# Optimization experiments

Hardware: AMD Instinct MI355X
Metric: run time of the kernel (lower is better)

Reference implementation:

```python
import jax, jax.numpy as jnp
import numpy as np

N, D, E, OUT = 50000, 256, 320000, 1

def setup_inputs() -> dict:
    key = jax.random.key(0)
    k1, k2, k3, k4, k5, k6 = jax.random.split(key, 6)
    z = jax.random.normal(k1, (N, D), dtype=jnp.float32)
    edge_index = jax.random.randint(k2, (2, E), 0, N, dtype=jnp.int64)
    # xavier_normal for fc1: std = sqrt(2/(fan_in+fan_out)) = sqrt(2/(2D+D))
    w1 = jax.random.normal(k3, (D, 2 * D), dtype=jnp.float32) * np.sqrt(2.0 / (3 * D))
    b1 = jnp.zeros((D,), dtype=jnp.float32)
    w2 = jax.random.normal(k4, (OUT, D), dtype=jnp.float32) * np.sqrt(2.0 / (D + OUT))
    b2 = jnp.zeros((OUT,), dtype=jnp.float32)
    return {"z": z, "edge_index": edge_index, "w1": w1, "b1": b1, "w2": w2, "b2": b2}

def reference(z, edge_index, w1, b1, w2, b2):
    x1 = z[edge_index[0]]                     # [E, D]
    x2 = z[edge_index[1]]                     # [E, D]
    x = jnp.concatenate([x1, x2], axis=1)     # [E, 2D]
    h = jax.nn.relu(x @ w1.T + b1)            # [E, D]
    return h @ w2.T + b2                      # [E, OUT]
```

## Files before the change

### kernel.cpp

```cpp
#include <hip/hip_runtime.h>
#include <hip/hip_bf16.h>

#define D 256
#define TWOD 512
#define BM 128
#define BK 32

typedef __attribute__((ext_vector_type(8))) __bf16 bf16x8;
typedef __attribute__((ext_vector_type(4))) float f32x4;
typedef __attribute__((ext_vector_type(8))) unsigned short ushort8;

using as1_u32 = __attribute__((address_space(1))) const unsigned int;
using as3_u32 = __attribute__((address_space(3))) unsigned int;

__device__ __forceinline__ void gload_lds16(const void* g, void* l) {
    __builtin_amdgcn_global_load_lds((as1_u32*)g, (as3_u32*)l, 16, 0, 0);
}

__device__ __forceinline__ float bf2f(unsigned short u) {
    unsigned int x = ((unsigned int)u) << 16;
    return __uint_as_float(x);
}
__device__ __forceinline__ unsigned short f2bf_bits(float f) {
    unsigned int x = __float_as_uint(f);
    unsigned int r = (x + 0x7fffu + ((x >> 16) & 1u)) >> 16;
    return (unsigned short)r;
}

__global__ __launch_bounds__(256) void wt_conv_kernel(
    const float* __restrict__ w1, unsigned short* __restrict__ Wt)
{
    const int s = blockIdx.x * 256 + threadIdx.x;
    const int j = s >> 9;
    const int kk = s & 511;
    const float v = w1[s];
    const int dst = (kk < D) ? (j * D + kk) : ((D + j) * D + (kk - D));
    Wt[dst] = f2bf_bits(v);
}

__global__ __launch_bounds__(256, 2) void node_proj_mfma(
    const float* __restrict__ z, const unsigned short* __restrict__ Wt,
    unsigned short* __restrict__ C, int M, int Mblocks)
{
    __shared__ __align__(16) float          Abuf[3][BM * BK];
    __shared__ __align__(16) unsigned short Bbuf[3][BM * BK];

    const int bid    = blockIdx.x;
    const int rowblk = (bid >> 5) * 8 + (bid & 7);
    if (rowblk >= Mblocks) return;
    const int m0 = rowblk * BM;
    const int cb = ((bid >> 3) & 3) * BM;

    const int t    = threadIdx.x;
    const int lane = t & 63;
    const int w    = t >> 6;

    const int r16 = lane & 15;
    const int g   = lane >> 4;

    const int wm = (w >> 1) * 64;
    const int wn = (w & 1) * 64;

    f32x4 acc[4][4];
    #pragma unroll
    for (int mt = 0; mt < 4; ++mt)
        #pragma unroll
        for (int nt = 0; nt < 4; ++nt)
            acc[mt][nt] = (f32x4){0.f, 0.f, 0.f, 0.f};

    auto stage = [&](int buf, int k0) {
        #pragma unroll
        for (int i = 0; i < 4; ++i) {
            const int c = i * 256 + t;
            const int r = c >> 3;
            const int q = c & 7;
            const int col = ((q ^ (r & 7)) << 2);
            const int row = min(m0 + r, M - 1);
            const float* gsrc = z + (size_t)row * D + k0 + col;
            float* ldst = &Abuf[buf][(size_t)(i * 256 + w * 64) * 4];
            gload_lds16(gsrc, ldst);
        }
        #pragma unroll
        for (int i = 0; i < 2; ++i) {
            const int c = i * 256 + t;
            const int r = c >> 2;
            const int q = c & 3;
            const int sb = (r ^ (r >> 2)) & 3;
            const int col = ((q ^ sb) << 3);
            const unsigned short* gsrc = Wt + (size_t)(cb + r) * D + k0 + col;
            unsigned short* ldst = &Bbuf[buf][(size_t)(i * 256 + w * 64) * 8];
            gload_lds16(gsrc, ldst);
        }
    };

    auto compute = [&](int buf) {
        bf16x8 b[4];
        #pragma unroll
        for (int nt = 0; nt < 4; ++nt) {
            const int rl = wn + nt * 16 + r16;
            const int sb = (rl ^ (rl >> 2)) & 3;
            const ushort8 bu = *(const ushort8*)&Bbuf[buf][rl * 32 + ((g ^ sb) << 3)];
            b[nt] = __builtin_bit_cast(bf16x8, bu);
        }
        bf16x8 a[4];
        #pragma unroll
        for (int mt = 0; mt < 4; ++mt) {
            const int rl = wm + mt * 16 + r16;
            const int s = rl & 7;
            const f32x4 f0 = *(const f32x4*)&Abuf[buf][rl * 32 + (((2 * g) ^ s) << 2)];
            const f32x4 f1 = *(const f32x4*)&Abuf[buf][rl * 32 + (((2 * g + 1) ^ s) << 2)];
            bf16x8 tt;
            tt[0] = (__bf16)f0[0]; tt[1] = (__bf16)f0[1];
            tt[2] = (__bf16)f0[2]; tt[3] = (__bf16)f0[3];
            tt[4] = (__bf16)f1[0]; tt[5] = (__bf16)f1[1];
            tt[6] = (__bf16)f1[2]; tt[7] = (__bf16)f1[3];
            a[mt] = tt;
        }

        __builtin_amdgcn_s_setprio(1);
        #pragma unroll
        for (int nt = 0; nt < 4; ++nt)
            #pragma unroll
            for (int mt = 0; mt < 4; ++mt)
                acc[mt][nt] = __builtin_amdgcn_mfma_f32_16x16x32_bf16(
                    b[nt], a[mt], acc[mt][nt], 0, 0, 0);
        __builtin_amdgcn_s_setprio(0);
    };

    stage(0, 0);
    stage(1, BK);

    #pragma unroll
    for (int kt = 0; kt < 7; ++kt) {
        asm volatile("s_waitcnt vmcnt(6)" ::: "memory");
        asm volatile("s_barrier" ::: "memory");
        if (kt + 2 < 8) stage((kt + 2) % 3, (kt + 2) * BK);
        compute(kt % 3);
    }
    asm volatile("s_waitcnt vmcnt(0)" ::: "memory");
    asm volatile("s_barrier" ::: "memory");
    compute(7 % 3);

    #pragma unroll
    for (int mt = 0; mt < 4; ++mt) {
        const int row = m0 + wm + mt * 16 + r16;
        if (row < M) {
            #pragma unroll
            for (int nt = 0; nt < 4; ++nt) {
                const int col = cb + wn + nt * 16 + g * 4;
                ushort4 pk;
                pk.x = f2bf_bits(acc[mt][nt][0]);
                pk.y = f2bf_bits(acc[mt][nt][1]);
                pk.z = f2bf_bits(acc[mt][nt][2]);
                pk.w = f2bf_bits(acc[mt][nt][3]);
                *(ushort4*)(C + (size_t)row * TWOD + col) = pk;
            }
        }
    }
}

__global__ __launch_bounds__(256) void edge_kernel(
    const int* __restrict__ ei, const unsigned short* __restrict__ C,
    const float* __restrict__ b1, const float* __restrict__ w2,
    const float* __restrict__ b2, float* __restrict__ out, int E)
{
    const int h   = threadIdx.x & 31;
    const int gid = (blockIdx.x * blockDim.x + threadIdx.x) >> 5;
    const int ng  = (gridDim.x * blockDim.x) >> 5;
    const int j0  = h * 8;

    const float4 w2a = *(const float4*)(w2 + j0);
    const float4 w2b = *(const float4*)(w2 + j0 + 4);
    const float4 b1a = *(const float4*)(b1 + j0);
    const float4 b1b = *(const float4*)(b1 + j0 + 4);
    const float  b2s = b2[0];

    auto dot8 = [&](const ushort8& ua, const ushort8& ub) -> float {
        float s;
        s  = fmaxf(bf2f(ua[0]) + bf2f(ub[0]) + b1a.x, 0.f) * w2a.x;
        s += fmaxf(bf2f(ua[1]) + bf2f(ub[1]) + b1a.y, 0.f) * w2a.y;
        s += fmaxf(bf2f(ua[2]) + bf2f(ub[2]) + b1a.z, 0.f) * w2a.z;
        s += fmaxf(bf2f(ua[3]) + bf2f(ub[3]) + b1a.w, 0.f) * w2a.w;
        s += fmaxf(bf2f(ua[4]) + bf2f(ub[4]) + b1b.x, 0.f) * w2b.x;
        s += fmaxf(bf2f(ua[5]) + bf2f(ub[5]) + b1b.y, 0.f) * w2b.y;
        s += fmaxf(bf2f(ua[6]) + bf2f(ub[6]) + b1b.z, 0.f) * w2b.z;
        s += fmaxf(bf2f(ua[7]) + bf2f(ub[7]) + b1b.w, 0.f) * w2b.w;
        return s;
    };

    int e = gid;
    for (; e + 3 * ng < E; e += 4 * ng) {
        const int e1 = e + ng, e2 = e + 2 * ng, e3 = e + 3 * ng;
        const int u0 = ei[e],  v0 = ei[E + e];
        const int u1 = ei[e1], v1 = ei[E + e1];
        const int u2 = ei[e2], v2 = ei[E + e2];
        const int u3 = ei[e3], v3 = ei[E + e3];

        const ushort8 ua0 = *(const ushort8*)(C + (size_t)u0 * TWOD + j0);
        const ushort8 ub0 = *(const ushort8*)(C + (size_t)v0 * TWOD + D + j0);
        const ushort8 ua1 = *(const ushort8*)(C + (size_t)u1 * TWOD + j0);
        const ushort8 ub1 = *(const ushort8*)(C + (size_t)v1 * TWOD + D + j0);
        const ushort8 ua2 = *(const ushort8*)(C + (size_t)u2 * TWOD + j0);
        const ushort8 ub2 = *(const ushort8*)(C + (size_t)v2 * TWOD + D + j0);
        const ushort8 ua3 = *(const ushort8*)(C + (size_t)u3 * TWOD + j0);
        const ushort8 ub3 = *(const ushort8*)(C + (size_t)v3 * TWOD + D + j0);

        float s0 = dot8(ua0, ub0);
        float s1 = dot8(ua1, ub1);
        float s2 = dot8(ua2, ub2);
        float s3 = dot8(ua3, ub3);

        #pragma unroll
        for (int off = 16; off; off >>= 1) {
            s0 += __shfl_xor(s0, off);
            s1 += __shfl_xor(s1, off);
            s2 += __shfl_xor(s2, off);
            s3 += __shfl_xor(s3, off);
        }

        if (h == 0) {
            out[e]  = s0 + b2s;
            out[e1] = s1 + b2s;
            out[e2] = s2 + b2s;
            out[e3] = s3 + b2s;
        }
    }
    for (; e < E; e += ng) {
        const int u = ei[e], v = ei[E + e];
        const ushort8 ua = *(const ushort8*)(C + (size_t)u * TWOD + j0);
        const ushort8 ub = *(const ushort8*)(C + (size_t)v * TWOD + D + j0);
        float s = dot8(ua, ub);
        #pragma unroll
        for (int off = 16; off; off >>= 1)
            s += __shfl_xor(s, off);
        if (h == 0) out[e] = s + b2s;
    }
}

extern "C" void kernel_launch(void* const* d_in, const int* in_sizes, int n_in,
                              void* d_out, int out_size, void* d_ws, size_t ws_size,
                              hipStream_t stream) {
    const float* z  = (const float*)d_in[0];
    const int*   ei = (const int*)d_in[1];
    const float* w1 = (const float*)d_in[2];
    const float* b1 = (const float*)d_in[3];
    const float* w2 = (const float*)d_in[4];
    const float* b2 = (const float*)d_in[5];
    float* out = (float*)d_out;

    const int M = in_sizes[0] / D;
    const int E = in_sizes[1] / 2;

    unsigned short* C  = (unsigned short*)d_ws;
    unsigned short* Wt = (unsigned short*)d_out;

    wt_conv_kernel<<<512, 256, 0, stream>>>(w1, Wt);

    const int Mblocks = (M + BM - 1) / BM;
    const int stripes = (Mblocks + 7) / 8;
    node_proj_mfma<<<stripes * 32, 256, 0, stream>>>(z, Wt, C, M, Mblocks);

    edge_kernel<<<4096, 256, 0, stream>>>(ei, C, b1, w2, b2, out, E);
}
```

Baseline: 93.38 us.

## Make node projection persistent with half of W1 resident in LDS

Replaces the tiled node-projection GEMM with a persistent kernel of 256 blocks of 512 threads. Each block loads half of the bf16 weight matrix (128 KB) into LDS once, then loops over 64-row tiles of z, streaming only A through a triple buffer. The weight conversion kernel now writes W in an MFMA-fragment-packed layout, so B reads become contiguous per lane without swizzling. This removes repeated weight reloads per tile, but one block per CU with a single 16-byte A load per thread per k-step may expose z-load latency and reduce occupancy.

Result: slower. 109.5 us (+17.3%).

```diff
diff --git a/kernel.cpp b/kernel.cpp
--- a/kernel.cpp
+++ b/kernel.cpp
@@ -3,8 +3,6 @@
 
 #define D 256
 #define TWOD 512
-#define BM 128
-#define BK 32
 
 typedef __attribute__((ext_vector_type(8))) __bf16 bf16x8;
 typedef __attribute__((ext_vector_type(4))) float f32x4;
@@ -28,132 +26,134 @@
 }
 
 __global__ __launch_bounds__(256) void wt_conv_kernel(
-    const float* __restrict__ w1, unsigned short* __restrict__ Wt)
+    const float* __restrict__ w1, unsigned short* __restrict__ WtP)
 {
     const int s = blockIdx.x * 256 + threadIdx.x;
-    const int j = s >> 9;
-    const int kk = s & 511;
+    const int o = s >> 9;
+    const int i = s & 511;
     const float v = w1[s];
-    const int dst = (kk < D) ? (j * D + kk) : ((D + j) * D + (kk - D));
-    Wt[dst] = f2bf_bits(v);
-}
-
-__global__ __launch_bounds__(256, 2) void node_proj_mfma(
-    const float* __restrict__ z, const unsigned short* __restrict__ Wt,
-    unsigned short* __restrict__ C, int M, int Mblocks)
+    const int jj = (i < D) ? o : (D + o);
+    const int k  = (i < D) ? i : (i - D);
+    const int c16 = jj >> 4, r = jj & 15;
+    const int kblk = k >> 5, kin = k & 31;
+    const int g = kin >> 3, kj = kin & 7;
+    WtP[(size_t)((c16 * 8 + kblk) * 512 + (r + 16 * g) * 8 + kj)] = f2bf_bits(v);
+}
+
+__global__ __launch_bounds__(512, 2) void node_proj_persist(
+    const float* __restrict__ z, const unsigned short* __restrict__ WtP,
+    unsigned short* __restrict__ C, int M, int NRT)
 {
-    __shared__ __align__(16) float          Abuf[3][BM * BK];
-    __shared__ __align__(16) unsigned short Bbuf[3][BM * BK];
-
-    const int bid    = blockIdx.x;
-    const int rowblk = (bid >> 5) * 8 + (bid & 7);
-    if (rowblk >= Mblocks) return;
-    const int m0 = rowblk * BM;
-    const int cb = ((bid >> 3) & 3) * BM;
-
+    __shared__ __align__(16) unsigned short Wlds[65536];
+    __shared__ __align__(16) float Abuf[3][64 * 32];
+
+    const int bid  = blockIdx.x;
+    const int ch   = bid & 1;
+    const int rt0  = bid >> 1;
     const int t    = threadIdx.x;
     const int lane = t & 63;
     const int w    = t >> 6;
-
-    const int r16 = lane & 15;
-    const int g   = lane >> 4;
-
-    const int wm = (w >> 1) * 64;
-    const int wn = (w & 1) * 64;
-
-    f32x4 acc[4][4];
-    #pragma unroll
-    for (int mt = 0; mt < 4; ++mt)
-        #pragma unroll
-        for (int nt = 0; nt < 4; ++nt)
-            acc[mt][nt] = (f32x4){0.f, 0.f, 0.f, 0.f};
-
-    auto stage = [&](int buf, int k0) {
-        #pragma unroll
-        for (int i = 0; i < 4; ++i) {
-            const int c = i * 256 + t;
-            const int r = c >> 3;
-            const int q = c & 7;
-            const int col = ((q ^ (r & 7)) << 2);
-            const int row = min(m0 + r, M - 1);
-            const float* gsrc = z + (size_t)row * D + k0 + col;
-            float* ldst = &Abuf[buf][(size_t)(i * 256 + w * 64) * 4];
-            gload_lds16(gsrc, ldst);
-        }
-        #pragma unroll
-        for (int i = 0; i < 2; ++i) {
-            const int c = i * 256 + t;
-            const int r = c >> 2;
-            const int q = c & 3;
-            const int sb = (r ^ (r >> 2)) & 3;
-            const int col = ((q ^ sb) << 3);
-            const unsigned short* gsrc = Wt + (size_t)(cb + r) * D + k0 + col;
-            unsigned short* ldst = &Bbuf[buf][(size_t)(i * 256 + w * 64) * 8];
-            gload_lds16(gsrc, ldst);
-        }
+    const int r16  = lane & 15;
+    const int g    = lane >> 4;
+
+    const int njobs = (NRT - 1 - rt0) / 128 + 1;
+    const int S = njobs * 8;
+
+    {
+        const unsigned short* src = WtP + (size_t)ch * 65536;
+        #pragma unroll
+        for (int i = 0; i < 16; ++i) {
+            const int chunk = i * 512 + t;
+            gload_lds16(src + (size_t)chunk * 8,
+                        &Wlds[(size_t)(i * 512 + w * 64) * 8]);
+        }
+    }
+
+    auto stageA = [&](int buf, int s) {
+        const int rt = rt0 + (s >> 3) * 128;
+        const int k0 = (s & 7) * 32;
+        const int r = t >> 3, q = t & 7;
+        const int col = (q ^ (r & 7)) << 2;
+        const int row = min(rt * 64 + r, M - 1);
+        gload_lds16(z + (size_t)row * D + k0 + col,
+                    &Abuf[buf][w * 256]);
     };
 
-    auto compute = [&](int buf) {
-        bf16x8 b[4];
-        #pragma unroll
-        for (int nt = 0; nt < 4; ++nt) {
-            const int rl = wn + nt * 16 + r16;
-            const int sb = (rl ^ (rl >> 2)) & 3;
-            const ushort8 bu = *(const ushort8*)&Bbuf[buf][rl * 32 + ((g ^ sb) << 3)];
-            b[nt] = __builtin_bit_cast(bf16x8, bu);
-        }
-        bf16x8 a[4];
+    stageA(0, 0);
+    if (1 < S) stageA(1, 1);
+
+    int flat = 0, bufc = 0;
+    for (int j = 0; j < njobs; ++j) {
+        const int rt = rt0 + j * 128;
+
+        f32x4 acc[4][2];
+        #pragma unroll
+        for (int mt = 0; mt < 4; ++mt)
+            #pragma unroll
+            for (int nt = 0; nt < 2; ++nt)
+                acc[mt][nt] = (f32x4){0.f, 0.f, 0.f, 0.f};
+
+        #pragma unroll
+        for (int kt = 0; kt < 8; ++kt) {
+            if (flat + 1 == S) asm volatile("s_waitcnt vmcnt(0)" ::: "memory");
+            else               asm volatile("s_waitcnt vmcnt(1)" ::: "memory");
+            __builtin_amdgcn_s_barrier();
+
+            const int s2 = flat + 2;
+            if (s2 < S) {
+                int buf2 = bufc + 2; if (buf2 >= 3) buf2 -= 3;
+                stageA(buf2, s2);
+            }
+
+            bf16x8 b[2];
+            #pragma unroll
+            for (int nt = 0; nt < 2; ++nt) {
+                const ushort8 bu = *(const ushort8*)
+                    &Wlds[(size_t)(((w * 2 + nt) * 8 + kt) * 512) + lane * 8];
+                b[nt] = __builtin_bit_cast(bf16x8, bu);
+            }
+            bf16x8 a[4];
+            #pragma unroll
+            for (int mt = 0; mt < 4; ++mt) {
+                const int rl = mt * 16 + r16;
+                const int sw = rl & 7;
+                const f32x4 f0 = *(const f32x4*)&Abuf[bufc][rl * 32 + (((2 * g) ^ sw) << 2)];
+                const f32x4 f1 = *(const f32x4*)&Abuf[bufc][rl * 32 + (((2 * g + 1) ^ sw) << 2)];
+                bf16x8 tt;
+                tt[0] = (__bf16)f0[0]; tt[1] = (__bf16)f0[1];
+                tt[2] = (__bf16)f0[2]; tt[3] = (__bf16)f0[3];
+                tt[4] = (__bf16)f1[0]; tt[5] = (__bf16)f1[1];
+                tt[6] = (__bf16)f1[2]; tt[7] = (__bf16)f1[3];
+                a[mt] = tt;
+            }
+
+            __builtin_amdgcn_s_setprio(1);
+            #pragma unroll
+            for (int nt = 0; nt < 2; ++nt)
+                #pragma unroll
+                for (int mt = 0; mt < 4; ++mt)
+                    acc[mt][nt] = __builtin_amdgcn_mfma_f32_16x16x32_bf16(
+                        b[nt], a[mt], acc[mt][nt], 0, 0, 0);
+            __builtin_amdgcn_s_setprio(0);
+
+            ++flat;
+            if (++bufc == 3) bufc = 0;
+        }
+
         #pragma unroll
         for (int mt = 0; mt < 4; ++mt) {
-            const int rl = wm + mt * 16 + r16;
-            const int s = rl & 7;
-            const f32x4 f0 = *(const f32x4*)&Abuf[buf][rl * 32 + (((2 * g) ^ s) << 2)];
-            const f32x4 f1 = *(const f32x4*)&Abuf[buf][rl * 32 + (((2 * g + 1) ^ s) << 2)];
-            bf16x8 tt;
-            tt[0] = (__bf16)f0[0]; tt[1] = (__bf16)f0[1];
-            tt[2] = (__bf16)f0[2]; tt[3] = (__bf16)f0[3];
-            tt[4] = (__bf16)f1[0]; tt[5] = (__bf16)f1[1];
-            tt[6] = (__bf16)f1[2]; tt[7] = (__bf16)f1[3];
-            a[mt] = tt;
-        }
-
-        __builtin_amdgcn_s_setprio(1);
-        #pragma unroll
-        for (int nt = 0; nt < 4; ++nt)
-            #pragma unroll
-            for (int mt = 0; mt < 4; ++mt)
-                acc[mt][nt] = __builtin_amdgcn_mfma_f32_16x16x32_bf16(
-                    b[nt], a[mt], acc[mt][nt], 0, 0, 0);
-        __builtin_amdgcn_s_setprio(0);
-    };
-
-    stage(0, 0);
-    stage(1, BK);
-
-    #pragma unroll
-    for (int kt = 0; kt < 7; ++kt) {
-        asm volatile("s_waitcnt vmcnt(6)" ::: "memory");
-        asm volatile("s_barrier" ::: "memory");
-        if (kt + 2 < 8) stage((kt + 2) % 3, (kt + 2) * BK);
-        compute(kt % 3);
-    }
-    asm volatile("s_waitcnt vmcnt(0)" ::: "memory");
-    asm volatile("s_barrier" ::: "memory");
-    compute(7 % 3);
-
-    #pragma unroll
-    for (int mt = 0; mt < 4; ++mt) {
-        const int row = m0 + wm + mt * 16 + r16;
-        if (row < M) {
-            #pragma unroll
-            for (int nt = 0; nt < 4; ++nt) {
-                const int col = cb + wn + nt * 16 + g * 4;
-                ushort4 pk;
-                pk.x = f2bf_bits(acc[mt][nt][0]);
-                pk.y = f2bf_bits(acc[mt][nt][1]);
-                pk.z = f2bf_bits(acc[mt][nt][2]);
-                pk.w = f2bf_bits(acc[mt][nt][3]);
-                *(ushort4*)(C + (size_t)row * TWOD + col) = pk;
+            const int row = rt * 64 + mt * 16 + r16;
+            if (row < M) {
+                #pragma unroll
+                for (int nt = 0; nt < 2; ++nt) {
+                    const int col = ch * 256 + w * 32 + nt * 16 + g * 4;
+                    ushort4 pk;
+                    pk.x = f2bf_bits(acc[mt][nt][0]);
+                    pk.y = f2bf_bits(acc[mt][nt][1]);
+                    pk.z = f2bf_bits(acc[mt][nt][2]);
+                    pk.w = f2bf_bits(acc[mt][nt][3]);
+                    *(ushort4*)(C + (size_t)row * TWOD + col) = pk;
+                }
             }
         }
     }
@@ -251,14 +251,13 @@
     const int M = in_sizes[0] / D;
     const int E = in_sizes[1] / 2;
 
-    unsigned short* C  = (unsigned short*)d_ws;
-    unsigned short* Wt = (unsigned short*)d_out;
-
-    wt_conv_kernel<<<512, 256, 0, stream>>>(w1, Wt);
-
-    const int Mblocks = (M + BM - 1) / BM;
-    const int stripes = (Mblocks + 7) / 8;
-    node_proj_mfma<<<stripes * 32, 256, 0, stream>>>(z, Wt, C, M, Mblocks);
+    unsigned short* C   = (unsigned short*)d_ws;
+    unsigned short* WtP = (unsigned short*)d_out;
+
+    wt_conv_kernel<<<512, 256, 0, stream>>>(w1, WtP);
+
+    const int NRT = (M + 63) / 64;
+    node_proj_persist<<<256, 512, 0, stream>>>(z, WtP, C, M, NRT);
 
     edge_kernel<<<4096, 256, 0, stream>>>(ei, C, b1, w2, b2, out, E);
 }
```

## Pre-pack weights in MFMA fragment order and load B directly from global

Applied to the files above, without the earlier changes.

The weight conversion kernel now writes W1 in a layout that matches the MFMA B-fragment, so each lane can read its 8 bf16 values with one contiguous 16-byte global load. B therefore no longer goes through LDS. It is double-buffered in registers one k-step ahead, and the wait counts change to match. LDS use drops to the A buffers only, and the launch bound is raised to 3 blocks per CU to allow more occupancy. The risk is that global/L2 latency on B loads may not be hidden, and register pressure rises with the occupancy target.

Measured after the change: 88.03 us. 1.06x faster.

```diff
diff --git a/kernel.cpp b/kernel.cpp
--- a/kernel.cpp
+++ b/kernel.cpp
@@ -28,22 +28,25 @@
 }
 
 __global__ __launch_bounds__(256) void wt_conv_kernel(
-    const float* __restrict__ w1, unsigned short* __restrict__ Wt)
+    const float* __restrict__ w1, unsigned short* __restrict__ WtP)
 {
     const int s = blockIdx.x * 256 + threadIdx.x;
-    const int j = s >> 9;
-    const int kk = s & 511;
+    const int o = s >> 9;
+    const int i = s & 511;
     const float v = w1[s];
-    const int dst = (kk < D) ? (j * D + kk) : ((D + j) * D + (kk - D));
-    Wt[dst] = f2bf_bits(v);
-}
-
-__global__ __launch_bounds__(256, 2) void node_proj_mfma(
-    const float* __restrict__ z, const unsigned short* __restrict__ Wt,
+    const int jj = (i < D) ? o : (D + o);
+    const int k  = (i < D) ? i : (i - D);
+    const int c16 = jj >> 4, r = jj & 15;
+    const int kblk = k >> 5, kin = k & 31;
+    const int g = kin >> 3, kj = kin & 7;
+    WtP[(size_t)((c16 * 8 + kblk) * 512 + (r + 16 * g) * 8 + kj)] = f2bf_bits(v);
+}
+
+__global__ __launch_bounds__(256, 3) void node_proj_mfma(
+    const float* __restrict__ z, const unsigned short* __restrict__ WtP,
     unsigned short* __restrict__ C, int M, int Mblocks)
 {
-    __shared__ __align__(16) float          Abuf[3][BM * BK];
-    __shared__ __align__(16) unsigned short Bbuf[3][BM * BK];
+    __shared__ __align__(16) float Abuf[3][BM * BK];
 
     const int bid    = blockIdx.x;
     const int rowblk = (bid >> 5) * 8 + (bid & 7);
@@ -60,6 +63,7 @@
 
     const int wm = (w >> 1) * 64;
     const int wn = (w & 1) * 64;
+    const int c16b = (cb + wn) >> 4;
 
     f32x4 acc[4][4];
     #pragma unroll
@@ -68,7 +72,7 @@
         for (int nt = 0; nt < 4; ++nt)
             acc[mt][nt] = (f32x4){0.f, 0.f, 0.f, 0.f};
 
-    auto stage = [&](int buf, int k0) {
+    auto stageA = [&](int buf, int k0) {
         #pragma unroll
         for (int i = 0; i < 4; ++i) {
             const int c = i * 256 + t;
@@ -80,35 +84,40 @@
             float* ldst = &Abuf[buf][(size_t)(i * 256 + w * 64) * 4];
             gload_lds16(gsrc, ldst);
         }
-        #pragma unroll
-        for (int i = 0; i < 2; ++i) {
-            const int c = i * 256 + t;
-            const int r = c >> 2;
-            const int q = c & 3;
-            const int sb = (r ^ (r >> 2)) & 3;
-            const int col = ((q ^ sb) << 3);
-            const unsigned short* gsrc = Wt + (size_t)(cb + r) * D + k0 + col;
-            unsigned short* ldst = &Bbuf[buf][(size_t)(i * 256 + w * 64) * 8];
-            gload_lds16(gsrc, ldst);
-        }
     };
 
-    auto compute = [&](int buf) {
-        bf16x8 b[4];
+    bf16x8 bb[2][4];
+    auto loadB = [&](int par, int kt) {
         #pragma unroll
         for (int nt = 0; nt < 4; ++nt) {
-            const int rl = wn + nt * 16 + r16;
-            const int sb = (rl ^ (rl >> 2)) & 3;
-            const ushort8 bu = *(const ushort8*)&Bbuf[buf][rl * 32 + ((g ^ sb) << 3)];
-            b[nt] = __builtin_bit_cast(bf16x8, bu);
-        }
+            const ushort8 bu = *(const ushort8*)(
+                WtP + (size_t)(((c16b + nt) * 8 + kt) * 512 + lane * 8));
+            bb[par][nt] = __builtin_bit_cast(bf16x8, bu);
+        }
+    };
+
+    stageA(0, 0);
+    stageA(1, BK);
+    __builtin_amdgcn_sched_barrier(0);
+    loadB(0, 0);
+
+    #pragma unroll
+    for (int kt = 0; kt < 8; ++kt) {
+        if (kt == 0 || kt == 7) asm volatile("s_waitcnt vmcnt(8)" ::: "memory");
+        else                    asm volatile("s_waitcnt vmcnt(12)" ::: "memory");
+        __builtin_amdgcn_s_barrier();
+
+        if (kt < 6) stageA((kt + 2) % 3, (kt + 2) * BK);
+        __builtin_amdgcn_sched_barrier(0);
+        if (kt < 7) loadB((kt + 1) & 1, kt + 1);
+
         bf16x8 a[4];
         #pragma unroll
         for (int mt = 0; mt < 4; ++mt) {
             const int rl = wm + mt * 16 + r16;
-            const int s = rl & 7;
-            const f32x4 f0 = *(const f32x4*)&Abuf[buf][rl * 32 + (((2 * g) ^ s) << 2)];
-            const f32x4 f1 = *(const f32x4*)&Abuf[buf][rl * 32 + (((2 * g + 1) ^ s) << 2)];
+            const int sw = rl & 7;
+            const f32x4 f0 = *(const f32x4*)&Abuf[kt % 3][rl * 32 + (((2 * g) ^ sw) << 2)];
+            const f32x4 f1 = *(const f32x4*)&Abuf[kt % 3][rl * 32 + (((2 * g + 1) ^ sw) << 2)];
             bf16x8 tt;
             tt[0] = (__bf16)f0[0]; tt[1] = (__bf16)f0[1];
             tt[2] = (__bf16)f0[2]; tt[3] = (__bf16)f0[3];
@@ -123,23 +132,9 @@
             #pragma unroll
             for (int mt = 0; mt < 4; ++mt)
                 acc[mt][nt] = __builtin_amdgcn_mfma_f32_16x16x32_bf16(
-                    b[nt], a[mt], acc[mt][nt], 0, 0, 0);
+                    bb[kt & 1][nt], a[mt], acc[mt][nt], 0, 0, 0);
         __builtin_amdgcn_s_setprio(0);
-    };
-
-    stage(0, 0);
-    stage(1, BK);
-
-    #pragma unroll
-    for (int kt = 0; kt < 7; ++kt) {
-        asm volatile("s_waitcnt vmcnt(6)" ::: "memory");
-        asm volatile("s_barrier" ::: "memory");
-        if (kt + 2 < 8) stage((kt + 2) % 3, (kt + 2) * BK);
-        compute(kt % 3);
-    }
-    asm volatile("s_waitcnt vmcnt(0)" ::: "memory");
-    asm volatile("s_barrier" ::: "memory");
-    compute(7 % 3);
+    }
 
     #pragma unroll
     for (int mt = 0; mt < 4; ++mt) {
@@ -251,14 +246,14 @@
     const int M = in_sizes[0] / D;
     const int E = in_sizes[1] / 2;
 
-    unsigned short* C  = (unsigned short*)d_ws;
-    unsigned short* Wt = (unsigned short*)d_out;
-
-    wt_conv_kernel<<<512, 256, 0, stream>>>(w1, Wt);
+    unsigned short* C   = (unsigned short*)d_ws;
+    unsigned short* WtP = (unsigned short*)d_out;
+
+    wt_conv_kernel<<<512, 256, 0, stream>>>(w1, WtP);
 
     const int Mblocks = (M + BM - 1) / BM;
     const int stripes = (Mblocks + 7) / 8;
-    node_proj_mfma<<<stripes * 32, 256, 0, stream>>>(z, Wt, C, M, Mblocks);
+    node_proj_mfma<<<stripes * 32, 256, 0, stream>>>(z, WtP, C, M, Mblocks);
 
     edge_kernel<<<4096, 256, 0, stream>>>(ei, C, b1, w2, b2, out, E);
 }
```
